# Kernel optimization log

Measured on AMD Instinct MI355X. Metric: run time of the kernel, lower is better.

## Reference

```python
import jax, jax.numpy as jnp
import numpy as np

N, F, C = 4096, 512, 512
NUM_HOPS, TOP_K, MASK_RATIO = 3, 8, 0.5
EPS = 1e-12


def setup_inputs() -> dict:
    key = jax.random.key(0)
    ks = jax.random.split(key, 8)
    return {
        "x": jax.random.normal(ks[0], (N, F), dtype=jnp.float32),
        "adj": jax.random.uniform(ks[1], (NUM_HOPS, N, N), dtype=jnp.float32),
        "rand_mask": jax.random.uniform(ks[2], (NUM_HOPS, N, N), dtype=jnp.float32),
        "W_in": jax.random.normal(ks[3], (F, C), dtype=jnp.float32) * 0.02,
        "b_in": jnp.zeros((C,), dtype=jnp.float32),
        "W_out": jax.random.normal(ks[4], (C, C), dtype=jnp.float32) * 0.02,
        "b_out": jnp.zeros((C,), dtype=jnp.float32),
        "alpha": jnp.ones((NUM_HOPS,), dtype=jnp.float32),
        "beta": jnp.full((1,), 0.5, dtype=jnp.float32),
    }


def reference(x, adj, rand_mask, W_in, b_in, W_out, b_out, alpha, beta):
    H_low = x @ W_in + b_in  # (N, C)
    # F.normalize(x, dim=-1) @ F.normalize(x.T, dim=0) == x_n @ x_n.T
    xn = x / jnp.maximum(jnp.linalg.norm(x, axis=-1, keepdims=True), EPS)
    sim = xn @ xn.T  # (N, N)
    a = jax.nn.softmax(alpha)
    rows = jnp.arange(N)[:, None]
    H_high = jnp.zeros((N, F), dtype=x.dtype)
    for k in range(NUM_HOPS):
        Akw = a[k] * adj[k] * sim  # (N, N)
        _, idx = jax.lax.top_k(Akw, TOP_K)  # (N, TOP_K)
        topk_mask = jnp.zeros_like(Akw).at[rows, idx].set(1.0)
        retain = (rand_mask[k] < MASK_RATIO).astype(Akw.dtype)
        final_mask = ((topk_mask + retain) > 0).astype(Akw.dtype)
        Hk = (Akw * final_mask) @ x  # (N, F)
        H_high = H_high + a[k] * Hk
    b = beta[0]
    H = jax.nn.relu(b * H_low + (1.0 - b) * H_high)
    # dropout in eval mode (identity)
    out = H @ W_out + b_out
    return jax.nn.log_softmax(out, axis=-1)
```

## Files before the change

### kernel.cpp

```cpp
#include <hip/hip_runtime.h>
#include <hip/hip_bf16.h>
#include <stdint.h>

#define NROW 4096
#define FDIM 512

typedef short bf16x8 __attribute__((ext_vector_type(8)));
typedef float f32x4 __attribute__((ext_vector_type(4)));
typedef float f4 __attribute__((ext_vector_type(4)));
typedef ushort u16x4 __attribute__((ext_vector_type(4)));

#define NEG_INF (-__builtin_inff())

__device__ inline ushort f2bf(float f) {
    union { float f; uint32_t u; } c{f};
    uint32_t u = c.u;
    uint32_t r = (u + 0x7FFF + ((u >> 16) & 1)) >> 16;
    return (ushort)r;
}
__device__ inline float bf2f(ushort h) {
    union { uint32_t u; float f; } c{((uint32_t)h) << 16};
    return c.f;
}
__device__ inline uint32_t cvt_pk_bf16(float lo, float hi) {
    uint32_t r;
    asm("v_cvt_pk_bf16_f32 %0, %1, %2" : "=v"(r) : "v"(lo), "v"(hi));
    return r;
}
__device__ inline float up0(uint32_t p) {
    union { uint32_t u; float f; } c{p << 16}; return c.f;
}
__device__ inline float up1(uint32_t p) {
    union { uint32_t u; float f; } c{p & 0xFFFF0000u}; return c.f;
}

__device__ inline float waveReduceMax(float v) {
    #pragma unroll
    for (int o = 32; o > 0; o >>= 1) v = fmaxf(v, __shfl_xor(v, o));
    return v;
}
__device__ inline float waveReduceSum(float v) {
    #pragma unroll
    for (int o = 32; o > 0; o >>= 1) v += __shfl_xor(v, o);
    return v;
}

__device__ inline void CE(float& a, float& b) {
    float mx = fmaxf(a, b);
    b = fminf(a, b);
    a = mx;
}
__device__ inline void sort8(float (&l)[8]) {
    CE(l[0],l[1]); CE(l[2],l[3]); CE(l[4],l[5]); CE(l[6],l[7]);
    CE(l[0],l[2]); CE(l[1],l[3]); CE(l[4],l[6]); CE(l[5],l[7]);
    CE(l[1],l[2]); CE(l[5],l[6]);
    CE(l[0],l[4]); CE(l[1],l[5]); CE(l[2],l[6]); CE(l[3],l[7]);
    CE(l[2],l[4]); CE(l[3],l[5]);
    CE(l[1],l[2]); CE(l[3],l[4]); CE(l[5],l[6]);
}
__device__ inline void mergeTop8(float (&a)[8], const float (&b)[8]) {
    float t[8];
    #pragma unroll
    for (int i = 0; i < 8; i++) t[i] = fmaxf(a[i], b[7 - i]);
    CE(t[0],t[4]); CE(t[1],t[5]); CE(t[2],t[6]); CE(t[3],t[7]);
    CE(t[0],t[2]); CE(t[1],t[3]); CE(t[4],t[6]); CE(t[5],t[7]);
    CE(t[0],t[1]); CE(t[2],t[3]); CE(t[4],t[5]); CE(t[6],t[7]);
    #pragma unroll
    for (int i = 0; i < 8; i++) a[i] = t[i];
}
__device__ inline float merge8th(const float (&a)[8], const float (&b)[8]) {
    float t0 = fminf(fmaxf(a[0], b[7]), fmaxf(a[1], b[6]));
    float t1 = fminf(fmaxf(a[2], b[5]), fmaxf(a[3], b[4]));
    float t2 = fminf(fmaxf(a[4], b[3]), fmaxf(a[5], b[2]));
    float t3 = fminf(fmaxf(a[6], b[1]), fmaxf(a[7], b[0]));
    return fminf(fminf(t0, t1), fminf(t2, t3));
}

#define GLL16(src, dst)                                                        \
    __builtin_amdgcn_global_load_lds(                                          \
        (const __attribute__((address_space(1))) void*)(src),                  \
        (__attribute__((address_space(3))) void*)(dst), 16, 0, 0)

__global__ __launch_bounds__(64) void coef_k(const float* __restrict__ alpha,
                                             const float* __restrict__ beta,
                                             float* __restrict__ coef) {
    if (threadIdx.x == 0) {
        float a0 = alpha[0], a1 = alpha[1], a2 = alpha[2];
        float m = fmaxf(a0, fmaxf(a1, a2));
        float e0 = expf(a0 - m), e1 = expf(a1 - m), e2 = expf(a2 - m);
        float s = e0 + e1 + e2;
        coef[0] = e0 / s; coef[1] = e1 / s; coef[2] = e2 / s;
        coef[3] = beta[0];
    }
}

__global__ __launch_bounds__(256) void prep_fused(
    const float* __restrict__ x, ushort* __restrict__ xn,
    ushort* __restrict__ xb, ushort* __restrict__ xbT,
    const float* __restrict__ W_in, ushort* __restrict__ WinT,
    const float* __restrict__ W_out, ushort* __restrict__ WoutT) {
    const int b = blockIdx.x;
    const int tid = threadIdx.x;
    __shared__ float b4[4];
    __shared__ ushort t[64][65];

    if (b < 4096) {
        const int row = b;
        int lane = tid & 63, w = tid >> 6;
        const float* xr = x + (size_t)row * FDIM;
        float v0 = xr[tid], v1 = xr[tid + 256];
        float ss = v0 * v0 + v1 * v1;
        ss = waveReduceSum(ss);
        if (lane == 0) b4[w] = ss;
        __syncthreads();
        float tot = b4[0] + b4[1] + b4[2] + b4[3];
        float inv = 1.f / fmaxf(sqrtf(tot), 1e-12f);
        size_t o = (size_t)row * FDIM + tid;
        xn[o] = f2bf(v0 * inv);  xn[o + 256] = f2bf(v1 * inv);
        xb[o] = f2bf(v0);        xb[o + 256] = f2bf(v1);
    } else if (b < 4608) {
        const int tb = b - 4096;
        const int c0 = (tb & 7) * 64, r0 = (tb >> 3) * 64;
        int lx = tid & 63, ly = tid >> 6;
        #pragma unroll
        for (int i = 0; i < 16; i++)
            t[ly + 4 * i][lx] = f2bf(x[(size_t)(r0 + ly + 4 * i) * FDIM + c0 + lx]);
        __syncthreads();
        #pragma unroll
        for (int i = 0; i < 16; i++)
            xbT[(size_t)(c0 + ly + 4 * i) * NROW + r0 + lx] = t[lx][ly + 4 * i];
    } else {
        const int cb = b - 4608;
        const float* Wf = (cb >> 6) ? W_out : W_in;
        ushort* WT = (cb >> 6) ? WoutT : WinT;
        const int idx = cb & 63;
        const int c0 = (idx & 7) * 64, r0 = (idx >> 3) * 64;
        int lx = tid & 63, ly = tid >> 6;
        #pragma unroll
        for (int i = 0; i < 16; i++)
            t[ly + 4 * i][lx] = f2bf(Wf[(size_t)(r0 + ly + 4 * i) * 512 + c0 + lx]);
        __syncthreads();
        #pragma unroll
        for (int i = 0; i < 16; i++)
            WT[(size_t)(c0 + ly + 4 * i) * 512 + r0 + lx] = t[lx][ly + 4 * i];
    }
}

__global__ __launch_bounds__(256) void gemm_sym(
    const ushort* __restrict__ A, ushort* __restrict__ C) {
    constexpr int BK = 64;
    constexpr int NT = 128 * BK;
    __shared__ __align__(16) ushort smem[128 * 130];
    ushort* As = smem;
    ushort* Bs = smem + NT;

    int bi = 0, rem = blockIdx.x;
    while (rem >= 32 - bi) { rem -= 32 - bi; bi++; }
    const int bj = bi + rem;
    const int m0 = bi * 128, n0 = bj * 128;

    const int tid = threadIdx.x;
    const int lane = tid & 63, w = tid >> 6;
    const int wr = w >> 1, wc = w & 1;

    f32x4 acc[4][4];
    #pragma unroll
    for (int mi = 0; mi < 4; mi++)
        #pragma unroll
        for (int ni = 0; ni < 4; ni++)
            #pragma unroll
            for (int r = 0; r < 4; r++) acc[mi][ni][r] = 0.f;

    for (int k0 = 0; k0 < FDIM; k0 += BK) {
        #pragma unroll
        for (int p = 0; p < 4; ++p) {
            int chunk = p * 256 + tid;
            int row = chunk / 8;
            int kc = chunk % 8;
            GLL16(A + (size_t)(m0 + row) * FDIM + k0 + kc * 8,
                  As + (size_t)(p * 256 + w * 64) * 8);
            GLL16(A + (size_t)(n0 + row) * FDIM + k0 + kc * 8,
                  Bs + (size_t)(p * 256 + w * 64) * 8);
        }
        __syncthreads();
        #pragma unroll
        for (int kf = 0; kf < BK / 32; ++kf) {
            const int ko = kf * 32 + (lane >> 4) * 8;
            bf16x8 av[4], bv[4];
            #pragma unroll
            for (int mi = 0; mi < 4; mi++)
                av[mi] = *(const bf16x8*)&As[(wr * 64 + mi * 16 + (lane & 15)) * BK + ko];
            #pragma unroll
            for (int ni = 0; ni < 4; ni++)
                bv[ni] = *(const bf16x8*)&Bs[(wc * 64 + ni * 16 + (lane & 15)) * BK + ko];
            #pragma unroll
            for (int mi = 0; mi < 4; mi++)
                #pragma unroll
                for (int ni = 0; ni < 4; ni++)
                    acc[mi][ni] = __builtin_amdgcn_mfma_f32_16x16x32_bf16(
                        av[mi], bv[ni], acc[mi][ni], 0, 0, 0);
        }
        __syncthreads();
    }

    #pragma unroll
    for (int mi = 0; mi < 4; mi++) {
        #pragma unroll
        for (int ni = 0; ni < 4; ni++) {
            int lcol = wc * 64 + ni * 16 + (lane & 15);
            #pragma unroll
            for (int r = 0; r < 4; r++) {
                int lrow = wr * 64 + mi * 16 + (lane >> 4) * 4 + r;
                ushort hv = f2bf(acc[mi][ni][r]);
                C[(size_t)(m0 + lrow) * NROW + n0 + lcol] = hv;
                smem[lrow * 130 + lcol] = hv;
            }
        }
    }

    if (bi != bj) {
        __syncthreads();
        const int wv = w;
        #pragma unroll 4
        for (int i = 0; i < 32; i++) {
            int r2 = wv * 32 + i;
            ushort a = smem[(lane * 2) * 130 + r2];
            ushort bb = smem[(lane * 2 + 1) * 130 + r2];
            uint32_t pk = (uint32_t)a | ((uint32_t)bb << 16);
            *(uint32_t*)&C[(size_t)(n0 + r2) * NROW + m0 + lane * 2] = pk;
        }
    }
}

template <int EPI>
__global__ __launch_bounds__(256) void gemm_abT(
    const ushort* __restrict__ A, int lda,
    const ushort* __restrict__ B, int ldb,
    int Kdim, int ldc,
    float* __restrict__ Cf, ushort* __restrict__ Pb,
    const float* __restrict__ bias,
    const ushort* __restrict__ A2, const ushort* __restrict__ B2,
    ushort* __restrict__ Pb4) {
    constexpr int BK = 64;
    constexpr int NT = 128 * BK;
    constexpr int CPR = BK / 8;
    constexpr int PASSES = (128 * CPR) / 256;
    __shared__ __align__(16) ushort smem[2 * NT];
    ushort* As = smem;
    ushort* Bs = smem + NT;

    int Kd = Kdim;
    if constexpr (EPI == 3) {
        if (blockIdx.z == 4) {
            A = A2; lda = FDIM; B = B2; ldb = FDIM; Kd = FDIM;
            Pb = Pb4;
        } else {
            A += (size_t)blockIdx.z * 1024;
            B += (size_t)blockIdx.z * 1024;
            Pb += (size_t)blockIdx.z * ((size_t)NROW * 512);
        }
    }

    const int tid = threadIdx.x;
    const int lane = tid & 63, w = tid >> 6;
    const int wr = w >> 1, wc = w & 1;
    const int m0 = blockIdx.y * 128;
    const int n0 = blockIdx.x * 128;

    f32x4 acc[4][4];
    #pragma unroll
    for (int mi = 0; mi < 4; mi++)
        #pragma unroll
        for (int ni = 0; ni < 4; ni++)
            #pragma unroll
            for (int r = 0; r < 4; r++) acc[mi][ni][r] = 0.f;

    for (int k0 = 0; k0 < Kd; k0 += BK) {
        #pragma unroll
        for (int p = 0; p < PASSES; ++p) {
            int chunk = p * 256 + tid;
            int row = chunk / CPR;
            int kc = chunk % CPR;
            const ushort* asrc = A + (size_t)(m0 + row) * lda + k0 + kc * 8;
            const ushort* bsrc = B + (size_t)(n0 + row) * ldb + k0 + kc * 8;
            ushort* abase = As + (size_t)(p * 256 + w * 64) * 8;
            ushort* bbase = Bs + (size_t)(p * 256 + w * 64) * 8;
            GLL16(asrc, abase);
            GLL16(bsrc, bbase);
        }
        __syncthreads();
        #pragma unroll
        for (int kf = 0; kf < BK / 32; ++kf) {
            const int ko = kf * 32 + (lane >> 4) * 8;
            bf16x8 av[4], bv[4];
            #pragma unroll
            for (int mi = 0; mi < 4; mi++)
                av[mi] = *(const bf16x8*)&As[(wr * 64 + mi * 16 + (lane & 15)) * BK + ko];
            #pragma unroll
            for (int ni = 0; ni < 4; ni++)
                bv[ni] = *(const bf16x8*)&Bs[(wc * 64 + ni * 16 + (lane & 15)) * BK + ko];
            #pragma unroll
            for (int mi = 0; mi < 4; mi++)
                #pragma unroll
                for (int ni = 0; ni < 4; ni++)
                    acc[mi][ni] = __builtin_amdgcn_mfma_f32_16x16x32_bf16(
                        av[mi], bv[ni], acc[mi][ni], 0, 0, 0);
        }
        __syncthreads();
    }

    #pragma unroll
    for (int mi = 0; mi < 4; mi++) {
        #pragma unroll
        for (int ni = 0; ni < 4; ni++) {
            int col = n0 + wc * 64 + ni * 16 + (lane & 15);
            #pragma unroll
            for (int r = 0; r < 4; r++) {
                int rowg = m0 + wr * 64 + mi * 16 + (lane >> 4) * 4 + r;
                size_t off = (size_t)rowg * ldc + col;
                float v = acc[mi][ni][r];
                if constexpr (EPI == 1) {
                    Cf[off] = v + bias[col];
                } else {
                    Pb[off] = f2bf(v);
                }
            }
        }
    }
}

__global__ __launch_bounds__(512) void topk_build_M(
    const ushort* __restrict__ simb, const float* __restrict__ adj,
    const float* __restrict__ rmask, const float* __restrict__ coef,
    ushort* __restrict__ Mout) {
    const int tid = threadIdx.x;
    const int lane = tid & 63;
    const int w = tid >> 6;
    const int rloc = w >> 2;
    const int wv = w & 3;
    const int row = blockIdx.x * 2 + rloc;
    __shared__ float wl[2][3][4][8];

    const int cbase = wv * 1024 + lane * 4;
    const size_t hopstride = (size_t)NROW * NROW;

    const ushort* srow = simb + (size_t)row * NROW + cbase;
    const float* arow = adj + (size_t)row * NROW + cbase;
    const float* rrow = rmask + (size_t)row * NROW + cbase;

    uint2 svp[4];
    #pragma unroll
    for (int q = 0; q < 4; q++)
        svp[q] = *(const uint2*)(srow + q * 256);

    float macc[4][4];
    #pragma unroll
    for (int q = 0; q < 4; q++)
        #pragma unroll
        for (int c = 0; c < 4; c++) macc[q][c] = 0.f;

    #pragma unroll 1
    for (int k = 0; k < 3; ++k) {
        const float* ar = arow + (size_t)k * hopstride;
        const float* rr = rrow + (size_t)k * hopstride;

        f4 rv[4], a[4];
        #pragma unroll
        for (int q = 0; q < 4; q++) rv[q] = *(const f4*)(rr + q * 256);
        #pragma unroll
        for (int q = 0; q < 4; q++) a[q] = *(const f4*)(ar + q * 256);

        uint32_t rbits = 0;
        #pragma unroll
        for (int q = 0; q < 4; q++) {
            rbits |= (rv[q].x < 0.5f ? 1u : 0u) << (q * 4 + 0);
            rbits |= (rv[q].y < 0.5f ? 1u : 0u) << (q * 4 + 1);
            rbits |= (rv[q].z < 0.5f ? 1u : 0u) << (q * 4 + 2);
            rbits |= (rv[q].w < 0.5f ? 1u : 0u) << (q * 4 + 3);
        }

        uint2 avp[4];
        #pragma unroll
        for (int q = 0; q < 4; q++) {
            avp[q].x = cvt_pk_bf16(a[q].x, a[q].y);
            avp[q].y = cvt_pk_bf16(a[q].z, a[q].w);
        }

        float lo8[8], hi8[8];
        #pragma unroll
        for (int qq = 0; qq < 2; qq++) {
            lo8[qq * 4 + 0] = up0(avp[qq].x) * up0(svp[qq].x);
            lo8[qq * 4 + 1] = up1(avp[qq].x) * up1(svp[qq].x);
            lo8[qq * 4 + 2] = up0(avp[qq].y) * up0(svp[qq].y);
            lo8[qq * 4 + 3] = up1(avp[qq].y) * up1(svp[qq].y);
        }
        #pragma unroll
        for (int qq = 0; qq < 2; qq++) {
            const int q = 2 + qq;
            hi8[qq * 4 + 0] = up0(avp[q].x) * up0(svp[q].x);
            hi8[qq * 4 + 1] = up1(avp[q].x) * up1(svp[q].x);
            hi8[qq * 4 + 2] = up0(avp[q].y) * up0(svp[q].y);
            hi8[qq * 4 + 3] = up1(avp[q].y) * up1(svp[q].y);
        }
        sort8(lo8);
        sort8(hi8);
        mergeTop8(lo8, hi8);

        #pragma unroll
        for (int lvl = 0; lvl < 6; lvl++) {
            float b[8];
            #pragma unroll
            for (int i = 0; i < 8; i++) b[i] = __shfl_xor(lo8[i], 1 << lvl);
            mergeTop8(lo8, b);
        }

        if (lane < 8) wl[rloc][k][wv][lane] = lo8[lane];
        __syncthreads();
        float b0[8], b1[8], b2[8];
        const int o0 = (wv + 1) & 3, o1 = (wv + 2) & 3, o2 = (wv + 3) & 3;
        #pragma unroll
        for (int i = 0; i < 8; i++) b0[i] = wl[rloc][k][o0][i];
        #pragma unroll
        for (int i = 0; i < 8; i++) b1[i] = wl[rloc][k][o1][i];
        #pragma unroll
        for (int i = 0; i < 8; i++) b2[i] = wl[rloc][k][o2][i];
        mergeTop8(lo8, b0);
        mergeTop8(lo8, b1);
        const float thr = merge8th(lo8, b2);

        const float ak = coef[k];
        const float aksq = ak * ak;
        #pragma unroll
        for (int q = 0; q < 4; q++) {
            float av0 = up0(avp[q].x), av1 = up1(avp[q].x);
            float av2 = up0(avp[q].y), av3 = up1(avp[q].y);
            float s0 = up0(svp[q].x), s1 = up1(svp[q].x);
            float s2 = up0(svp[q].y), s3 = up1(svp[q].y);
            bool m0 = ((rbits >> (q * 4 + 0)) & 1) || (av0 * s0 >= thr);
            bool m1 = ((rbits >> (q * 4 + 1)) & 1) || (av1 * s1 >= thr);
            bool m2 = ((rbits >> (q * 4 + 2)) & 1) || (av2 * s2 >= thr);
            bool m3 = ((rbits >> (q * 4 + 3)) & 1) || (av3 * s3 >= thr);
            macc[q][0] += m0 ? aksq * av0 : 0.f;
            macc[q][1] += m1 ? aksq * av1 : 0.f;
            macc[q][2] += m2 ? aksq * av2 : 0.f;
            macc[q][3] += m3 ? aksq * av3 : 0.f;
        }
    }

    ushort* mrow = Mout + (size_t)row * NROW + cbase;
    #pragma unroll
    for (int q = 0; q < 4; q++) {
        u16x4 o;
        o[0] = f2bf(up0(svp[q].x) * macc[q][0]);
        o[1] = f2bf(up1(svp[q].x) * macc[q][1]);
        o[2] = f2bf(up0(svp[q].y) * macc[q][2]);
        o[3] = f2bf(up1(svp[q].y) * macc[q][3]);
        *(u16x4*)(mrow + q * 256) = o;
    }
}

__global__ __launch_bounds__(256) void reduce_relu(
    const ushort* __restrict__ parts, const ushort* __restrict__ parts4,
    const float* __restrict__ bias, const float* __restrict__ coef,
    ushort* __restrict__ Hb) {
    const size_t i = (size_t)blockIdx.x * 256 + threadIdx.x;
    f4 s = {0.f, 0.f, 0.f, 0.f};
    #pragma unroll
    for (int z = 0; z < 4; z++) {
        u16x4 p = *((const u16x4*)parts + (size_t)z * 524288 + i);
        #pragma unroll
        for (int c = 0; c < 4; c++) s[c] += bf2f(p[c]);
    }
    u16x4 h4 = *((const u16x4*)parts4 + i);
    f4 bi = ((const f4*)bias)[i & 127];
    float cb = coef[3];
    u16x4 o;
    #pragma unroll
    for (int c = 0; c < 4; c++) {
        float h = cb * (bf2f(h4[c]) + bi[c]) + (1.f - cb) * s[c];
        o[c] = f2bf(fmaxf(h, 0.f));
    }
    *((u16x4*)Hb + i) = o;
}

__global__ __launch_bounds__(256) void logsoftmax_k(const float* __restrict__ L,
                                                    float* __restrict__ out) {
    int row = blockIdx.x, tid = threadIdx.x;
    int lane = tid & 63, w = tid >> 6;
    const float* lr = L + (size_t)row * 512;
    float v0 = lr[tid], v1 = lr[tid + 256];
    __shared__ float bm[4], bs[4];
    float m = fmaxf(v0, v1);
    m = waveReduceMax(m);
    if (lane == 0) bm[w] = m;
    __syncthreads();
    float M = fmaxf(fmaxf(bm[0], bm[1]), fmaxf(bm[2], bm[3]));
    float s = expf(v0 - M) + expf(v1 - M);
    s = waveReduceSum(s);
    if (lane == 0) bs[w] = s;
    __syncthreads();
    float S = bs[0] + bs[1] + bs[2] + bs[3];
    float lse = M + logf(S);
    float* orow = out + (size_t)row * 512;
    orow[tid] = v0 - lse;
    orow[tid + 256] = v1 - lse;
}

extern "C" void kernel_launch(void* const* d_in, const int* in_sizes, int n_in,
                              void* d_out, int out_size, void* d_ws, size_t ws_size,
                              hipStream_t stream) {
    const float* x     = (const float*)d_in[0];
    const float* adj   = (const float*)d_in[1];
    const float* rmask = (const float*)d_in[2];
    const float* W_in  = (const float*)d_in[3];
    const float* b_in  = (const float*)d_in[4];
    const float* W_out = (const float*)d_in[5];
    const float* b_out = (const float*)d_in[6];
    const float* alpha = (const float*)d_in[7];
    const float* beta  = (const float*)d_in[8];
    float* out = (float*)d_out;

    const size_t MB = 1024 * 1024;
    char* wsb = (char*)d_ws;
    ushort* simb   = (ushort*)wsb;
    ushort* parts  = (ushort*)wsb;
    ushort* parts4 = (ushort*)(wsb + 16 * MB);
    float*  logits = (float*)(wsb + 20 * MB);
    ushort* Mb     = (ushort*)(wsb + 32 * MB);
    ushort* xn     = (ushort*)(wsb + 64 * MB);
    ushort* xb     = (ushort*)(wsb + 68 * MB);
    ushort* xbT    = (ushort*)(wsb + 72 * MB);
    ushort* WinT   = (ushort*)(wsb + 76 * MB);
    ushort* WoutT  = (ushort*)(wsb + 76 * MB + 512 * 1024);
    ushort* Hb     = (ushort*)(wsb + 85 * MB);
    float*  coef   = (float*)(wsb + 89 * MB);

    coef_k<<<1, 64, 0, stream>>>(alpha, beta, coef);

    prep_fused<<<4096 + 512 + 128, 256, 0, stream>>>(
        x, xn, xb, xbT, W_in, WinT, W_out, WoutT);

    gemm_sym<<<528, 256, 0, stream>>>(xn, simb);

    topk_build_M<<<NROW / 2, 512, 0, stream>>>(simb, adj, rmask, coef, Mb);

    gemm_abT<3><<<dim3(4, 32, 5), 256, 0, stream>>>(
        Mb, NROW, xbT, NROW, 1024, 512, nullptr, parts, nullptr,
        xb, WinT, parts4);

    reduce_relu<<<2048, 256, 0, stream>>>(parts, parts4, b_in, coef, Hb);

    gemm_abT<1><<<dim3(4, 32), 256, 0, stream>>>(
        Hb, 512, WoutT, 512, 512, 512, logits, nullptr, b_out,
        nullptr, nullptr, nullptr);

    logsoftmax_k<<<NROW, 256, 0, stream>>>(logits, out);
}
```

Measured before the change: 204.9 us.

## Process one row per wavefront in top-k mask build, dropping LDS reduction

Measured after the change: 249.4 us. +21.7%, slower.

```diff
diff --git a/kernel.cpp b/kernel.cpp
--- a/kernel.cpp
+++ b/kernel.cpp
@@ -67,13 +67,6 @@
     CE(t[0],t[1]); CE(t[2],t[3]); CE(t[4],t[5]); CE(t[6],t[7]);
     #pragma unroll
     for (int i = 0; i < 8; i++) a[i] = t[i];
-}
-__device__ inline float merge8th(const float (&a)[8], const float (&b)[8]) {
-    float t0 = fminf(fmaxf(a[0], b[7]), fmaxf(a[1], b[6]));
-    float t1 = fminf(fmaxf(a[2], b[5]), fmaxf(a[3], b[4]));
-    float t2 = fminf(fmaxf(a[4], b[3]), fmaxf(a[5], b[2]));
-    float t3 = fminf(fmaxf(a[6], b[1]), fmaxf(a[7], b[0]));
-    return fminf(fminf(t0, t1), fminf(t2, t3));
 }
 
 #define GLL16(src, dst)                                                        \
@@ -329,133 +322,130 @@
     }
 }
 
-__global__ __launch_bounds__(512) void topk_build_M(
+__global__ __launch_bounds__(256) void topk_build_M(
     const ushort* __restrict__ simb, const float* __restrict__ adj,
     const float* __restrict__ rmask, const float* __restrict__ coef,
     ushort* __restrict__ Mout) {
-    const int tid = threadIdx.x;
-    const int lane = tid & 63;
-    const int w = tid >> 6;
-    const int rloc = w >> 2;
-    const int wv = w & 3;
-    const int row = blockIdx.x * 2 + rloc;
-    __shared__ float wl[2][3][4][8];
-
-    const int cbase = wv * 1024 + lane * 4;
-    const size_t hopstride = (size_t)NROW * NROW;
-
-    const ushort* srow = simb + (size_t)row * NROW + cbase;
-    const float* arow = adj + (size_t)row * NROW + cbase;
-    const float* rrow = rmask + (size_t)row * NROW + cbase;
-
-    uint2 svp[4];
-    #pragma unroll
-    for (int q = 0; q < 4; q++)
-        svp[q] = *(const uint2*)(srow + q * 256);
-
-    float macc[4][4];
-    #pragma unroll
-    for (int q = 0; q < 4; q++)
-        #pragma unroll
-        for (int c = 0; c < 4; c++) macc[q][c] = 0.f;
+    const int lane = threadIdx.x & 63;
+    const int w = threadIdx.x >> 6;
+    const int row = blockIdx.x * 4 + w;
+    const int loff = lane * 4;
+    const size_t hs = (size_t)NROW * NROW;
+
+    const ushort* srow = simb + (size_t)row * NROW + loff;
+    const float* arow = adj + (size_t)row * NROW + loff;
+    const float* rrow = rmask + (size_t)row * NROW + loff;
+
+    uint2 svp[16];
+    #pragma unroll
+    for (int i = 0; i < 16; i++) svp[i] = *(const uint2*)(srow + i * 256);
+
+    uint32_t mp[16][2];
+    #pragma unroll
+    for (int i = 0; i < 16; i++) { mp[i][0] = 0u; mp[i][1] = 0u; }
 
     #pragma unroll 1
     for (int k = 0; k < 3; ++k) {
-        const float* ar = arow + (size_t)k * hopstride;
-        const float* rr = rrow + (size_t)k * hopstride;
-
-        f4 rv[4], a[4];
-        #pragma unroll
-        for (int q = 0; q < 4; q++) rv[q] = *(const f4*)(rr + q * 256);
-        #pragma unroll
-        for (int q = 0; q < 4; q++) a[q] = *(const f4*)(ar + q * 256);
-
-        uint32_t rbits = 0;
-        #pragma unroll
-        for (int q = 0; q < 4; q++) {
-            rbits |= (rv[q].x < 0.5f ? 1u : 0u) << (q * 4 + 0);
-            rbits |= (rv[q].y < 0.5f ? 1u : 0u) << (q * 4 + 1);
-            rbits |= (rv[q].z < 0.5f ? 1u : 0u) << (q * 4 + 2);
-            rbits |= (rv[q].w < 0.5f ? 1u : 0u) << (q * 4 + 3);
-        }
-
-        uint2 avp[4];
-        #pragma unroll
-        for (int q = 0; q < 4; q++) {
-            avp[q].x = cvt_pk_bf16(a[q].x, a[q].y);
-            avp[q].y = cvt_pk_bf16(a[q].z, a[q].w);
-        }
-
-        float lo8[8], hi8[8];
-        #pragma unroll
-        for (int qq = 0; qq < 2; qq++) {
-            lo8[qq * 4 + 0] = up0(avp[qq].x) * up0(svp[qq].x);
-            lo8[qq * 4 + 1] = up1(avp[qq].x) * up1(svp[qq].x);
-            lo8[qq * 4 + 2] = up0(avp[qq].y) * up0(svp[qq].y);
-            lo8[qq * 4 + 3] = up1(avp[qq].y) * up1(svp[qq].y);
-        }
-        #pragma unroll
-        for (int qq = 0; qq < 2; qq++) {
-            const int q = 2 + qq;
-            hi8[qq * 4 + 0] = up0(avp[q].x) * up0(svp[q].x);
-            hi8[qq * 4 + 1] = up1(avp[q].x) * up1(svp[q].x);
-            hi8[qq * 4 + 2] = up0(avp[q].y) * up0(svp[q].y);
-            hi8[qq * 4 + 3] = up1(avp[q].y) * up1(svp[q].y);
-        }
-        sort8(lo8);
-        sort8(hi8);
-        mergeTop8(lo8, hi8);
+        const float* ar = arow + (size_t)k * hs;
+        const float* rr = rrow + (size_t)k * hs;
+
+        uint2 avp[16];
+        uint32_t rb[2] = {0u, 0u};
+        float run[8];
+
+        #pragma unroll 2
+        for (int g = 0; g < 4; ++g) {
+            f4 rv[4], a[4];
+            #pragma unroll
+            for (int i = 0; i < 4; i++)
+                rv[i] = *(const f4*)(rr + (g * 4 + i) * 256);
+            #pragma unroll
+            for (int i = 0; i < 4; i++)
+                a[i] = *(const f4*)(ar + (g * 4 + i) * 256);
+
+            #pragma unroll
+            for (int i = 0; i < 4; i++) {
+                const int bit = (g * 4 + i) * 4 & 31;
+                uint32_t bits = (rv[i].x < 0.5f ? 1u : 0u)
+                              | (rv[i].y < 0.5f ? 2u : 0u)
+                              | (rv[i].z < 0.5f ? 4u : 0u)
+                              | (rv[i].w < 0.5f ? 8u : 0u);
+                rb[g >> 1] |= bits << bit;
+            }
+            #pragma unroll
+            for (int i = 0; i < 4; i++) {
+                avp[g * 4 + i].x = cvt_pk_bf16(a[i].x, a[i].y);
+                avp[g * 4 + i].y = cvt_pk_bf16(a[i].z, a[i].w);
+            }
+
+            float t[8], u[8];
+            #pragma unroll
+            for (int i = 0; i < 2; i++) {
+                const int q = g * 4 + i;
+                t[i * 4 + 0] = up0(avp[q].x) * up0(svp[q].x);
+                t[i * 4 + 1] = up1(avp[q].x) * up1(svp[q].x);
+                t[i * 4 + 2] = up0(avp[q].y) * up0(svp[q].y);
+                t[i * 4 + 3] = up1(avp[q].y) * up1(svp[q].y);
+            }
+            #pragma unroll
+            for (int i = 0; i < 2; i++) {
+                const int q = g * 4 + 2 + i;
+                u[i * 4 + 0] = up0(avp[q].x) * up0(svp[q].x);
+                u[i * 4 + 1] = up1(avp[q].x) * up1(svp[q].x);
+                u[i * 4 + 2] = up0(avp[q].y) * up0(svp[q].y);
+                u[i * 4 + 3] = up1(avp[q].y) * up1(svp[q].y);
+            }
+            sort8(t);
+            sort8(u);
+            mergeTop8(t, u);
+            if (g == 0) {
+                #pragma unroll
+                for (int i = 0; i < 8; i++) run[i] = t[i];
+            } else {
+                mergeTop8(run, t);
+            }
+        }
 
         #pragma unroll
         for (int lvl = 0; lvl < 6; lvl++) {
             float b[8];
             #pragma unroll
-            for (int i = 0; i < 8; i++) b[i] = __shfl_xor(lo8[i], 1 << lvl);
-            mergeTop8(lo8, b);
-        }
-
-        if (lane < 8) wl[rloc][k][wv][lane] = lo8[lane];
-        __syncthreads();
-        float b0[8], b1[8], b2[8];
-        const int o0 = (wv + 1) & 3, o1 = (wv + 2) & 3, o2 = (wv + 3) & 3;
-        #pragma unroll
-        for (int i = 0; i < 8; i++) b0[i] = wl[rloc][k][o0][i];
-        #pragma unroll
-        for (int i = 0; i < 8; i++) b1[i] = wl[rloc][k][o1][i];
-        #pragma unroll
-        for (int i = 0; i < 8; i++) b2[i] = wl[rloc][k][o2][i];
-        mergeTop8(lo8, b0);
-        mergeTop8(lo8, b1);
-        const float thr = merge8th(lo8, b2);
+            for (int i = 0; i < 8; i++) b[i] = __shfl_xor(run[i], 1 << lvl);
+            mergeTop8(run, b);
+        }
+        const float thr = run[7];
 
         const float ak = coef[k];
         const float aksq = ak * ak;
         #pragma unroll
-        for (int q = 0; q < 4; q++) {
-            float av0 = up0(avp[q].x), av1 = up1(avp[q].x);
-            float av2 = up0(avp[q].y), av3 = up1(avp[q].y);
-            float s0 = up0(svp[q].x), s1 = up1(svp[q].x);
-            float s2 = up0(svp[q].y), s3 = up1(svp[q].y);
-            bool m0 = ((rbits >> (q * 4 + 0)) & 1) || (av0 * s0 >= thr);
-            bool m1 = ((rbits >> (q * 4 + 1)) & 1) || (av1 * s1 >= thr);
-            bool m2 = ((rbits >> (q * 4 + 2)) & 1) || (av2 * s2 >= thr);
-            bool m3 = ((rbits >> (q * 4 + 3)) & 1) || (av3 * s3 >= thr);
-            macc[q][0] += m0 ? aksq * av0 : 0.f;
-            macc[q][1] += m1 ? aksq * av1 : 0.f;
-            macc[q][2] += m2 ? aksq * av2 : 0.f;
-            macc[q][3] += m3 ? aksq * av3 : 0.f;
-        }
-    }
-
-    ushort* mrow = Mout + (size_t)row * NROW + cbase;
-    #pragma unroll
-    for (int q = 0; q < 4; q++) {
+        for (int i = 0; i < 16; i++) {
+            float a0 = up0(avp[i].x), a1 = up1(avp[i].x);
+            float a2 = up0(avp[i].y), a3 = up1(avp[i].y);
+            float s0 = up0(svp[i].x), s1 = up1(svp[i].x);
+            float s2 = up0(svp[i].y), s3 = up1(svp[i].y);
+            const uint32_t bits = rb[i >> 3] >> ((i * 4) & 31);
+            bool m0 = (bits & 1) || (a0 * s0 >= thr);
+            bool m1 = (bits & 2) || (a1 * s1 >= thr);
+            bool m2 = (bits & 4) || (a2 * s2 >= thr);
+            bool m3 = (bits & 8) || (a3 * s3 >= thr);
+            float d0 = m0 ? aksq * a0 : 0.f;
+            float d1 = m1 ? aksq * a1 : 0.f;
+            float d2 = m2 ? aksq * a2 : 0.f;
+            float d3 = m3 ? aksq * a3 : 0.f;
+            mp[i][0] = cvt_pk_bf16(up0(mp[i][0]) + d0, up1(mp[i][0]) + d1);
+            mp[i][1] = cvt_pk_bf16(up0(mp[i][1]) + d2, up1(mp[i][1]) + d3);
+        }
+    }
+
+    ushort* mrow = Mout + (size_t)row * NROW + loff;
+    #pragma unroll
+    for (int i = 0; i < 16; i++) {
         u16x4 o;
-        o[0] = f2bf(up0(svp[q].x) * macc[q][0]);
-        o[1] = f2bf(up1(svp[q].x) * macc[q][1]);
-        o[2] = f2bf(up0(svp[q].y) * macc[q][2]);
-        o[3] = f2bf(up1(svp[q].y) * macc[q][3]);
-        *(u16x4*)(mrow + q * 256) = o;
+        o[0] = f2bf(up0(svp[i].x) * up0(mp[i][0]));
+        o[1] = f2bf(up1(svp[i].x) * up1(mp[i][0]));
+        o[2] = f2bf(up0(svp[i].y) * up0(mp[i][1]));
+        o[3] = f2bf(up1(svp[i].y) * up1(mp[i][1]));
+        *(u16x4*)(mrow + i * 256) = o;
     }
 }
 
@@ -542,7 +532,7 @@
 
     gemm_sym<<<528, 256, 0, stream>>>(xn, simb);
 
-    topk_build_M<<<NROW / 2, 512, 0, stream>>>(simb, adj, rmask, coef, Mb);
+    topk_build_M<<<NROW / 4, 256, 0, stream>>>(simb, adj, rmask, coef, Mb);
 
     gemm_abT<3><<<dim3(4, 32, 5), 256, 0, stream>>>(
         Mb, NROW, xbT, NROW, 1024, 512, nullptr, parts, nullptr,
```
